# Kernel tuning notes

Measured on AMD Instinct MI355X. Metric: run time of the kernel, lower is better.

The kernel has to match this reference:

```python
import jax, jax.numpy as jnp
import numpy as np

B, H, L, DIM = 4, 8, 1024, 256
D = DIM // H  # per-head dim
DEPTH, LAYER_I = 12, 1  # layer_index < depth//4 -> adjacency masking active


def _gcn(xh, adj, W):
    # One graph-convolution layer (GCN used as q/k/v projection in the repo):
    # support = x @ W per head, then aggregate with the (attention-)adjacency.
    # xh: [b,h,t,d], adj: [b,h,l,t], W: [d,d] -> [b,h,l,d]
    return jnp.einsum('bhlt,bhtd->bhld', adj, xh @ W)


def _split_heads(x):
    # 'b t (h d) -> b h t d'
    b, t, _ = x.shape
    return x.reshape(b, t, H, D).transpose(0, 2, 1, 3)


def _merge_heads(v):
    # 'b h t d -> b t (h d)'
    b, h, t, d = v.shape
    return v.transpose(0, 2, 1, 3).reshape(b, t, h * d)


def setup_inputs() -> dict:
    key = jax.random.key(0)
    ks = jax.random.split(key, 9)
    x = jax.random.normal(ks[0], (B, L, DIM), jnp.float32)
    resize_x = jax.random.normal(ks[1], (B, L, DIM), jnpp := jnp.float32) if False else jax.random.normal(ks[1], (B, L, DIM), jnp.float32)
    eye = jnp.eye(L, dtype=jnp.float32)[None, None]  # self-loops so no all-masked rows
    adj = jnp.clip((jax.random.uniform(ks[2], (B, H, L, L)) < 0.1).astype(jnp.float32) + eye, 0.0, 1.0)
    adj_resize = jnp.clip((jax.random.uniform(ks[3], (B, H, L, L)) < 0.1).astype(jnp.float32) + eye, 0.0, 1.0)
    s = D ** -0.5
    Wq = jax.random.normal(ks[4], (D, D), jnp.float32) * s
    Wk = jax.random.normal(ks[5], (D, D), jnp.float32) * s
    Wv = jax.random.normal(ks[6], (D, D), jnp.float32) * s
    R = jax.random.normal(ks[7], (H, H), jnp.float32)  # 'randomatrix' head-mixing param
    Wp = jax.random.normal(ks[8], (DIM, DIM), jnp.float32) * (DIM ** -0.5)  # proj_v (no bias)
    return {'x': x, 'resize_x': resize_x, 'adj': adj, 'adj_resize': adj_resize,
            'Wq': Wq, 'Wk': Wk, 'Wv': Wv, 'R': R, 'Wp': Wp}


def reference(x, resize_x, adj, adj_resize, Wq, Wk, Wv, R, Wp):
    scale = DIM ** -0.5  # note: torch code scales by dim**-0.5 (full dim, not d_head)
    xh = _split_heads(x)          # [b,h,l,d]
    rxh = _split_heads(resize_x)  # [b,h,t,d]
    q = _gcn(xh, adj, Wq)         # [b,h,l,d]
    k = _gcn(rxh, adj_resize, Wk)  # [b,h,t,d]
    attn = jnp.einsum('bhld,bhtd->bhlt', q, k) * scale
    attn = jax.nn.leaky_relu(attn, negative_slope=0.01)
    # cross-head mixing with learned HxH matrix: out[b,i] = sum_h R[i,h]*attn[b,h]
    attn = jnp.einsum('ih,bhlt->bilt', R, attn)
    if LAYER_I < DEPTH // 4:
        attn = jnp.where(adj > 0, attn, -jnp.inf)
    A = jax.nn.softmax(attn, axis=-1)                      # rep_adj
    Ar = jax.nn.softmax(A.transpose(0, 1, 3, 2), axis=-1)  # dual softmax on transpose
    v = _merge_heads(_gcn(xh, A, Wv))
    out = jax.nn.gelu(v, approximate=False) @ Wp
    vr = _merge_heads(_gcn(rxh, Ar, Wv))
    out_resize = jax.nn.gelu(vr, approximate=False) @ Wp
    return out, out_resize, A, Ar
```

## Files before the change

### kernel.cpp

```cpp
#include <hip/hip_runtime.h>
#include <hip/hip_bf16.h>
#include <math.h>

#define BB 4
#define HH 8
#define LL 1024
#define DD 32
#define DIMM 256

typedef unsigned short u16;
typedef unsigned int u32;
typedef short bf16x8 __attribute__((ext_vector_type(8)));
typedef float f32x4 __attribute__((ext_vector_type(4)));

__device__ __forceinline__ float bu2f(u16 s) {
  union { unsigned int u; float f; } cv; cv.u = ((unsigned int)s) << 16; return cv.f;
}
__device__ __forceinline__ u16 f2bu(float f) {
  union { float f; unsigned int u; } cv; cv.f = f;
  unsigned int u = cv.u;
  u += 0x7FFFu + ((u >> 16) & 1u);
  return (u16)(u >> 16);
}
__device__ __forceinline__ short f2bs(float f) {
  return (short)__bfloat16_as_ushort(__float2bfloat16(f));
}

__global__ __launch_bounds__(256) void k_proj(
    const float* __restrict__ x, const float* __restrict__ rx,
    const float* __restrict__ Wq, const float* __restrict__ Wk, const float* __restrict__ Wv,
    u16* __restrict__ xqT_hi, u16* __restrict__ xqT_lo,
    u16* __restrict__ xkT_hi, u16* __restrict__ xkT_lo,
    u16* __restrict__ xvT_hi, u16* __restrict__ xvrT_hi) {
  __shared__ float wq[32][32], wk[32][32], wv[32][32];
  __shared__ float xs[8][32], rxs[8][32];
  __shared__ float tq_[32][9], tk_[32][9], tv_[32][9], tvr_[32][9];
  int tid = threadIdx.x, bid = blockIdx.x;
  int chunk = bid & 127, h = (bid >> 7) & 7, b = bid >> 10;
  int t0 = chunk << 3;
  for (int i = tid; i < 1024; i += 256) {
    int r = i >> 5, c = i & 31;
    wq[r][c] = Wq[i]; wk[r][c] = Wk[i]; wv[r][c] = Wv[i];
  }
  int d = tid & 31, tl = tid >> 5;
  size_t xoff = ((size_t)b * LL + t0 + tl) * DIMM + h * 32 + d;
  xs[tl][d]  = x[xoff];
  rxs[tl][d] = rx[xoff];
  __syncthreads();
  float aq = 0.f, ak = 0.f, av = 0.f, ar = 0.f;
#pragma unroll
  for (int dp = 0; dp < 32; ++dp) {
    float xv_ = xs[tl][dp], rv_ = rxs[tl][dp];
    aq += xv_ * wq[dp][d];
    ak += rv_ * wk[dp][d];
    av += xv_ * wv[dp][d];
    ar += rv_ * wv[dp][d];
  }
  tq_[d][tl] = aq; tk_[d][tl] = ak; tv_[d][tl] = av; tvr_[d][tl] = ar;
  __syncthreads();
  int d2 = tid >> 3, t2 = tid & 7;
  size_t obase = ((size_t)((b * HH + h) * DD + d2)) * LL + t0 + t2;
  {
    float v = tq_[d2][t2]; u16 hi = f2bu(v);
    xqT_hi[obase] = hi; xqT_lo[obase] = f2bu(v - bu2f(hi));
  }
  {
    float v = tk_[d2][t2]; u16 hi = f2bu(v);
    xkT_hi[obase] = hi; xkT_lo[obase] = f2bu(v - bu2f(hi));
  }
  xvT_hi[obase]  = f2bu(tv_[d2][t2]);
  xvrT_hi[obase] = f2bu(tvr_[d2][t2]);
}

template<int PREC, int OUT_SPLIT, int WRITE_BITS>
__global__ __launch_bounds__(256) void k_wmat2(
    const float* __restrict__ wA, const float* __restrict__ wB,
    const u16* __restrict__ sAh, const u16* __restrict__ sAl,
    const u16* __restrict__ sBh, const u16* __restrict__ sBl,
    float* __restrict__ dA, float* __restrict__ dB,
    u16* __restrict__ dAhi, u16* __restrict__ dAlo,
    u16* __restrict__ dBhi, u16* __restrict__ dBlo,
    u32* __restrict__ bits) {
  int tid = threadIdx.x, bid = blockIdx.x;
  int sel = bid >> 9;
  const float* w  = sel ? wB : wA;
  const u16* sh   = sel ? sBh : sAh;
  const u16* sl   = sel ? sBl : sAl;
  float* dst      = sel ? dB : dA;
  u16* dhi        = sel ? dBhi : dAhi;
  u16* dlo        = sel ? dBlo : dAlo;
  int b2 = bid & 511;
  int lc = b2 & 15, bh = b2 >> 4;
  int wave = tid >> 6, lane = tid & 63;
  int l0 = (lc << 6) + (wave << 4);
  int col = lane & 15, g = lane >> 4;
  const float* wrow = w + ((size_t)bh * LL + l0 + col) * LL + (g << 3);
  const u16* b0h = sh + ((size_t)bh * DD + col) * LL + (g << 3);
  const u16* b1h = b0h + 16 * LL;
  const u16* b0l = PREC == 2 ? sl + ((size_t)bh * DD + col) * LL + (g << 3) : nullptr;
  const u16* b1l = PREC == 2 ? b0l + 16 * LL : nullptr;
  unsigned char* bytep = nullptr;
  if (WRITE_BITS && sel == 0)
    bytep = (unsigned char*)(bits + (size_t)bh * 32 * LL + l0 + col) + g;
  f32x4 acc0 = {0.f, 0.f, 0.f, 0.f}, acc1 = {0.f, 0.f, 0.f, 0.f};
#pragma unroll 2
  for (int t0 = 0; t0 < LL; t0 += 32) {
    f32x4 wa = *(const f32x4*)(wrow + t0);
    f32x4 wb = *(const f32x4*)(wrow + t0 + 4);
    bf16x8 whi;
#pragma unroll
    for (int i = 0; i < 4; ++i) {
      whi[i]     = f2bs(wa[i]);
      whi[i + 4] = f2bs(wb[i]);
    }
    if (WRITE_BITS && sel == 0) {
      unsigned int byte = 0;
#pragma unroll
      for (int i = 0; i < 4; ++i) {
        byte |= (wa[i] > 0.f ? 1u : 0u) << i;
        byte |= (wb[i] > 0.f ? 1u : 0u) << (4 + i);
      }
      bytep[(size_t)(t0 >> 5) * (LL * 4)] = (unsigned char)byte;
    }
    bf16x8 s0h = *(const bf16x8*)(b0h + t0);
    bf16x8 s1h = *(const bf16x8*)(b1h + t0);
    acc0 = __builtin_amdgcn_mfma_f32_16x16x32_bf16(whi, s0h, acc0, 0, 0, 0);
    acc1 = __builtin_amdgcn_mfma_f32_16x16x32_bf16(whi, s1h, acc1, 0, 0, 0);
    if (PREC == 2) {
      bf16x8 s0l = *(const bf16x8*)(b0l + t0);
      bf16x8 s1l = *(const bf16x8*)(b1l + t0);
      acc0 = __builtin_amdgcn_mfma_f32_16x16x32_bf16(whi, s0l, acc0, 0, 0, 0);
      acc1 = __builtin_amdgcn_mfma_f32_16x16x32_bf16(whi, s1l, acc1, 0, 0, 0);
    }
  }
#pragma unroll
  for (int i = 0; i < 4; ++i) {
    size_t o = ((size_t)bh * LL + l0 + (g << 2) + i) * DD;
    if (OUT_SPLIT) {
      float v0 = acc0[i]; u16 h0 = f2bu(v0);
      dhi[o + col] = h0; dlo[o + col] = f2bu(v0 - bu2f(h0));
      float v1 = acc1[i]; u16 h1 = f2bu(v1);
      dhi[o + 16 + col] = h1; dlo[o + 16 + col] = f2bu(v1 - bu2f(h1));
    } else {
      dst[o + col] = acc0[i];
      dst[o + 16 + col] = acc1[i];
    }
  }
}

__global__ __launch_bounds__(256) void k_logits_mfma(
    const u16* __restrict__ qh, const u16* __restrict__ ql,
    const u16* __restrict__ kh, const u16* __restrict__ kl,
    const float* __restrict__ Rm, const u32* __restrict__ bits,
    float* __restrict__ M) {
  __shared__ float Rlds[8][8];
  __shared__ float mtile[4][16 * 17];
  int tid = threadIdx.x, bid = blockIdx.x;
  int tb = bid & 7, lb = (bid >> 3) & 15, b = bid >> 7;
  int wave = tid >> 6, lane = tid & 63;
  int l0 = (lb << 6) + (wave << 4);
  int tbase = tb << 7;
  int idx16 = lane & 15, g = lane >> 4;
  if (tid < 64) Rlds[tid >> 3][tid & 7] = Rm[tid];
  bf16x8 qfh[8], qfl[8];
#pragma unroll
  for (int h = 0; h < 8; ++h) {
    size_t off = ((size_t)(b * HH + h) * LL + l0 + idx16) * DD + (g << 3);
    qfh[h] = *(const bf16x8*)(qh + off);
    qfl[h] = *(const bf16x8*)(ql + off);
  }
  __syncthreads();
  int rr_ = lane >> 2, c0 = (lane & 3) << 2;
  for (int tt = 0; tt < 8; ++tt) {
    int t = tbase + (tt << 4);
    f32x4 S[8];
#pragma unroll
    for (int h = 0; h < 8; ++h) {
      size_t koff = ((size_t)(b * HH + h) * LL + t + idx16) * DD + (g << 3);
      bf16x8 bh_ = *(const bf16x8*)(kh + koff);
      bf16x8 bl_ = *(const bf16x8*)(kl + koff);
      f32x4 s = {0.f, 0.f, 0.f, 0.f};
      s = __builtin_amdgcn_mfma_f32_16x16x32_bf16(qfh[h], bh_, s, 0, 0, 0);
      s = __builtin_amdgcn_mfma_f32_16x16x32_bf16(qfl[h], bh_, s, 0, 0, 0);
      s = __builtin_amdgcn_mfma_f32_16x16x32_bf16(qfh[h], bl_, s, 0, 0, 0);
      S[h] = s;
    }
#pragma unroll
    for (int h = 0; h < 8; ++h)
#pragma unroll
      for (int e = 0; e < 4; ++e) {
        float v = S[h][e] * 0.0625f;
        S[h][e] = (v > 0.f) ? v : 0.01f * v;
      }
    int word = t >> 5;
    int bitpos = ((tt & 1) << 4) + idx16;
#pragma unroll
    for (int i = 0; i < 8; ++i) {
      float rr8[8];
#pragma unroll
      for (int h = 0; h < 8; ++h) rr8[h] = Rlds[i][h];
      const u32* bp = bits + ((size_t)(b * HH + i) * 32 + word) * LL + l0 + (g << 2);
      u32 mw0 = bp[0], mw1 = bp[1], mw2 = bp[2], mw3 = bp[3];
      float m_[4];
#pragma unroll
      for (int e = 0; e < 4; ++e) {
        float acc = 0.f;
#pragma unroll
        for (int h = 0; h < 8; ++h) acc += rr8[h] * S[h][e];
        u32 mw = (e == 0) ? mw0 : (e == 1) ? mw1 : (e == 2) ? mw2 : mw3;
        m_[e] = ((mw >> bitpos) & 1u) ? acc : -INFINITY;
      }
#pragma unroll
      for (int e = 0; e < 4; ++e)
        mtile[wave][((g << 2) + e) * 17 + idx16] = m_[e];
      float4 v4;
      v4.x = mtile[wave][rr_ * 17 + c0 + 0];
      v4.y = mtile[wave][rr_ * 17 + c0 + 1];
      v4.z = mtile[wave][rr_ * 17 + c0 + 2];
      v4.w = mtile[wave][rr_ * 17 + c0 + 3];
      *(float4*)(M + ((size_t)(b * HH + i) * LL + l0 + rr_) * LL + t + c0) = v4;
    }
  }
}

__global__ __launch_bounds__(256) void k_norm2(
    float* __restrict__ A, float* __restrict__ colpart) {
  __shared__ float cacc[4][1024];
  int tid = threadIdx.x, bid = blockIdx.x;
  int ch = bid & 31, bh = bid >> 5;
  int wave = tid >> 6, lane = tid & 63;
  float4 colA[4];
#pragma unroll
  for (int j = 0; j < 4; ++j) colA[j] = make_float4(0.f, 0.f, 0.f, 0.f);
  for (int rr = 0; rr < 8; ++rr) {
    int l = (ch << 5) + (rr << 2) + wave;
    float4* Ap = (float4*)(A + ((size_t)bh * LL + l) * LL);
    float4 v[4];
#pragma unroll
    for (int j = 0; j < 4; ++j) v[j] = Ap[lane + (j << 6)];
    float mx = -INFINITY;
#pragma unroll
    for (int j = 0; j < 4; ++j)
      mx = fmaxf(mx, fmaxf(fmaxf(v[j].x, v[j].y), fmaxf(v[j].z, v[j].w)));
#pragma unroll
    for (int o = 32; o > 0; o >>= 1) mx = fmaxf(mx, __shfl_xor(mx, o, 64));
    float sm = 0.f;
#pragma unroll
    for (int j = 0; j < 4; ++j) {
      v[j].x = __expf(v[j].x - mx); v[j].y = __expf(v[j].y - mx);
      v[j].z = __expf(v[j].z - mx); v[j].w = __expf(v[j].w - mx);
      sm += v[j].x + v[j].y + v[j].z + v[j].w;
    }
#pragma unroll
    for (int o = 32; o > 0; o >>= 1) sm += __shfl_xor(sm, o, 64);
    float inv = 1.0f / sm;
#pragma unroll
    for (int j = 0; j < 4; ++j) {
      v[j].x *= inv; v[j].y *= inv; v[j].z *= inv; v[j].w *= inv;
      colA[j].x += __expf(v[j].x); colA[j].y += __expf(v[j].y);
      colA[j].z += __expf(v[j].z); colA[j].w += __expf(v[j].w);
      Ap[lane + (j << 6)] = v[j];
    }
  }
#pragma unroll
  for (int j = 0; j < 4; ++j)
    *(float4*)&cacc[wave][(j << 8) + (lane << 2)] = colA[j];
  __syncthreads();
  float4 s = make_float4(0.f, 0.f, 0.f, 0.f);
#pragma unroll
  for (int w = 0; w < 4; ++w) {
    float4 t = *(const float4*)&cacc[w][tid << 2];
    s.x += t.x; s.y += t.y; s.z += t.z; s.w += t.w;
  }
  ((float4*)(colpart + ((size_t)bh * 32 + ch) * LL))[tid] = s;
}

__global__ __launch_bounds__(256) void k_colred(
    const float* __restrict__ colpart, float* __restrict__ colsum) {
  int gid = blockIdx.x * 256 + threadIdx.x;
  int bh = gid >> 10, t = gid & 1023;
  const float* cp = colpart + (size_t)bh * 32 * LL + t;
  float s = 0.f;
#pragma unroll
  for (int c = 0; c < 32; ++c) s += cp[c * LL];
  colsum[gid] = s;
}

__global__ __launch_bounds__(256) void k_ar(
    const float* __restrict__ A, const float* __restrict__ colsum, float* __restrict__ Ar) {
  __shared__ float tile[64][65];
  int tid = threadIdx.x, bid = blockIdx.x;
  int tix = bid & 15, tiy = (bid >> 4) & 15, bh = bid >> 8;
  int l0 = tiy << 6, t0 = tix << 6;
  int c = tid & 63, r4 = tid >> 6;
  const float* Ab = A + ((size_t)bh * LL + l0) * LL + t0;
#pragma unroll
  for (int rr = 0; rr < 16; ++rr) {
    int li = (rr << 2) + r4;
    tile[li][c] = __expf(Ab[(size_t)li * LL + c]);
  }
  __syncthreads();
  float* Arb = Ar + ((size_t)bh * LL + t0) * LL + l0;
  const float* cs = colsum + bh * LL + t0;
#pragma unroll
  for (int rr = 0; rr < 16; ++rr) {
    int ti = (rr << 2) + r4;
    float inv = 1.0f / cs[ti];
    Arb[(size_t)ti * LL + c] = tile[c][ti] * inv;
  }
}

__global__ __launch_bounds__(256) void k_out2(
    const float* __restrict__ vb, const float* __restrict__ vrb,
    const float* __restrict__ Wp,
    float* __restrict__ out, float* __restrict__ outr) {
  __shared__ float g_s[16 * 256];
  __shared__ float wp_s[32 * 256];
  int tid = threadIdx.x, bid = blockIdx.x;
  int sel = bid >> 8;
  const float* vbuf = sel ? vrb : vb;
  float* o = sel ? outr : out;
  int b2 = bid & 255;
  int lt = b2 & 63, b = b2 >> 6;
  int l0 = lt << 4;
  int h = tid >> 5, dd = tid & 31;
#pragma unroll
  for (int r = 0; r < 16; ++r) {
    float v = vbuf[(((size_t)b * HH + h) * LL + l0 + r) * DD + dd];
    g_s[r * 256 + tid] = 0.5f * v * (1.0f + erff(v * 0.70710678118654752f));
  }
  float acc[16];
#pragma unroll
  for (int r = 0; r < 16; ++r) acc[r] = 0.f;
  for (int jc = 0; jc < 8; ++jc) {
    __syncthreads();
#pragma unroll
    for (int u = 0; u < 8; ++u) {
      int idx = tid + (u << 8);
      int j = idx >> 6, c4 = idx & 63;
      float4 v = *(const float4*)(Wp + (size_t)(jc * 32 + j) * DIMM + (c4 << 2));
      *(float4*)&wp_s[j * 256 + (c4 << 2)] = v;
    }
    __syncthreads();
#pragma unroll
    for (int j = 0; j < 32; ++j) {
      float wv = wp_s[j * 256 + tid];
      int jj = (jc << 5) + j;
#pragma unroll
      for (int r = 0; r < 16; ++r)
        acc[r] += g_s[r * 256 + jj] * wv;
    }
  }
#pragma unroll
  for (int r = 0; r < 16; ++r)
    o[((size_t)b * LL + l0 + r) * DIMM + tid] = acc[r];
}

extern "C" void kernel_launch(void* const* d_in, const int* in_sizes, int n_in,
                              void* d_out, int out_size, void* d_ws, size_t ws_size,
                              hipStream_t stream) {
  const float* x    = (const float*)d_in[0];
  const float* rx   = (const float*)d_in[1];
  const float* adj  = (const float*)d_in[2];
  const float* adjr = (const float*)d_in[3];
  const float* Wq   = (const float*)d_in[4];
  const float* Wk   = (const float*)d_in[5];
  const float* Wv   = (const float*)d_in[6];
  const float* Rm   = (const float*)d_in[7];
  const float* Wp   = (const float*)d_in[8];

  const size_t NE = (size_t)BB * HH * LL * DD;

  float* out  = (float*)d_out;
  float* outr = out + NE;
  float* A    = outr + NE;
  float* Ar   = A + (size_t)BB * HH * LL * LL;

  float* colpart = Ar;
  u16* q_hi   = (u16*)(Ar + NE);
  u16* q_lo   = q_hi + NE;
  u16* k_hi   = q_lo + NE;
  u16* k_lo   = k_hi + NE;
  u16* xqT_hi = k_lo + NE;
  u16* xqT_lo = xqT_hi + NE;
  u16* xkT_hi = xqT_lo + NE;
  u16* xkT_lo = xkT_hi + NE;
  u16* xvT_hi  = (u16*)out;
  u16* xvrT_hi = (u16*)outr;

  float* wsf    = (float*)d_ws;
  float* vb     = wsf;
  float* vrb    = wsf + NE;
  float* colsum = wsf + 2 * NE;
  u32* adjbits  = (u32*)(wsf + 2 * NE + 32768);

  k_proj<<<4096, 256, 0, stream>>>(x, rx, Wq, Wk, Wv,
                                   xqT_hi, xqT_lo, xkT_hi, xkT_lo,
                                   xvT_hi, xvrT_hi);
  k_wmat2<2,1,1><<<1024, 256, 0, stream>>>(adj, adjr,
                                           xqT_hi, xqT_lo, xkT_hi, xkT_lo,
                                           nullptr, nullptr,
                                           q_hi, q_lo, k_hi, k_lo, adjbits);
  k_logits_mfma<<<512, 256, 0, stream>>>(q_hi, q_lo, k_hi, k_lo, Rm, adjbits, A);
  k_norm2<<<1024, 256, 0, stream>>>(A, colpart);
  k_colred<<<128, 256, 0, stream>>>(colpart, colsum);
  k_ar<<<8192, 256, 0, stream>>>(A, colsum, Ar);
  k_wmat2<1,0,0><<<1024, 256, 0, stream>>>(A, Ar,
                                           xvT_hi, nullptr, xvrT_hi, nullptr,
                                           vb, vrb,
                                           nullptr, nullptr, nullptr, nullptr, nullptr);
  k_out2<<<512, 256, 0, stream>>>(vb, vrb, Wp, out, outr);
}
```

Baseline: 423.4 us.

## Fuse value aggregation GEMMs into softmax-normalize and transpose kernels

```diff
diff --git a/kernel.cpp b/kernel.cpp
--- a/kernel.cpp
+++ b/kernel.cpp
@@ -223,9 +223,10 @@
   }
 }
 
-__global__ __launch_bounds__(256) void k_norm2(
-    float* __restrict__ A, float* __restrict__ colpart) {
-  __shared__ float cacc[4][1024];
+__global__ __launch_bounds__(256) void k_norm2v(
+    float* __restrict__ A, const u16* __restrict__ xvT,
+    float* __restrict__ colpart, float* __restrict__ vb) {
+  __shared__ u16 Ast[32][1032];
   int tid = threadIdx.x, bid = blockIdx.x;
   int ch = bid & 31, bh = bid >> 5;
   int wave = tid >> 6, lane = tid & 63;
@@ -233,7 +234,8 @@
 #pragma unroll
   for (int j = 0; j < 4; ++j) colA[j] = make_float4(0.f, 0.f, 0.f, 0.f);
   for (int rr = 0; rr < 8; ++rr) {
-    int l = (ch << 5) + (rr << 2) + wave;
+    int row = (rr << 2) + wave;
+    int l = (ch << 5) + row;
     float4* Ap = (float4*)(A + ((size_t)bh * LL + l) * LL);
     float4 v[4];
 #pragma unroll
@@ -260,16 +262,35 @@
       colA[j].x += __expf(v[j].x); colA[j].y += __expf(v[j].y);
       colA[j].z += __expf(v[j].z); colA[j].w += __expf(v[j].w);
       Ap[lane + (j << 6)] = v[j];
-    }
-  }
+      int c4 = (lane + (j << 6)) << 2;
+      *(short4*)&Ast[row][c4] =
+          make_short4(f2bs(v[j].x), f2bs(v[j].y), f2bs(v[j].z), f2bs(v[j].w));
+    }
+  }
+  __syncthreads();
+  int idx16 = lane & 15, g = lane >> 4;
+  int Mt = wave >> 1, Nt = wave & 1;
+  f32x4 acc = {0.f, 0.f, 0.f, 0.f};
+  const u16* bbase = xvT + ((size_t)bh * DD + Nt * 16 + idx16) * LL;
+#pragma unroll 4
+  for (int kc = 0; kc < 32; ++kc) {
+    bf16x8 af = *(const bf16x8*)&Ast[(Mt << 4) + idx16][(kc << 5) + (g << 3)];
+    bf16x8 bfr = *(const bf16x8*)(bbase + (kc << 5) + (g << 3));
+    acc = __builtin_amdgcn_mfma_f32_16x16x32_bf16(af, bfr, acc, 0, 0, 0);
+  }
+#pragma unroll
+  for (int e = 0; e < 4; ++e)
+    vb[((size_t)bh * LL + (ch << 5) + (Mt << 4) + (g << 2) + e) * DD + Nt * 16 + idx16] = acc[e];
+  __syncthreads();
+  float* cf = (float*)&Ast[0][0];
 #pragma unroll
   for (int j = 0; j < 4; ++j)
-    *(float4*)&cacc[wave][(j << 8) + (lane << 2)] = colA[j];
+    *(float4*)&cf[wave * 1024 + (j << 8) + (lane << 2)] = colA[j];
   __syncthreads();
   float4 s = make_float4(0.f, 0.f, 0.f, 0.f);
 #pragma unroll
   for (int w = 0; w < 4; ++w) {
-    float4 t = *(const float4*)&cacc[w][tid << 2];
+    float4 t = *(const float4*)&cf[w * 1024 + (tid << 2)];
     s.x += t.x; s.y += t.y; s.z += t.z; s.w += t.w;
   }
   ((float4*)(colpart + ((size_t)bh * 32 + ch) * LL))[tid] = s;
@@ -286,27 +307,51 @@
   colsum[gid] = s;
 }
 
-__global__ __launch_bounds__(256) void k_ar(
-    const float* __restrict__ A, const float* __restrict__ colsum, float* __restrict__ Ar) {
+__global__ __launch_bounds__(256) void k_arv(
+    const float* __restrict__ A, const float* __restrict__ colsum,
+    const u16* __restrict__ xvrT, float* __restrict__ Ar, float* __restrict__ vrb) {
   __shared__ float tile[64][65];
   int tid = threadIdx.x, bid = blockIdx.x;
-  int tix = bid & 15, tiy = (bid >> 4) & 15, bh = bid >> 8;
-  int l0 = tiy << 6, t0 = tix << 6;
-  int c = tid & 63, r4 = tid >> 6;
-  const float* Ab = A + ((size_t)bh * LL + l0) * LL + t0;
-#pragma unroll
-  for (int rr = 0; rr < 16; ++rr) {
-    int li = (rr << 2) + r4;
-    tile[li][c] = __expf(Ab[(size_t)li * LL + c]);
-  }
-  __syncthreads();
-  float* Arb = Ar + ((size_t)bh * LL + t0) * LL + l0;
-  const float* cs = colsum + bh * LL + t0;
-#pragma unroll
-  for (int rr = 0; rr < 16; ++rr) {
-    int ti = (rr << 2) + r4;
-    float inv = 1.0f / cs[ti];
-    Arb[(size_t)ti * LL + c] = tile[c][ti] * inv;
+  int tix = bid & 15, bh = bid >> 4;
+  int t0 = tix << 6;
+  int c = tid & 63, w4 = tid >> 6;
+  int idx16 = c & 15, g = (c >> 4) & 3;
+  float invc = 1.0f / colsum[(size_t)bh * LL + t0 + c];
+  f32x4 acc0 = {0.f, 0.f, 0.f, 0.f}, acc1 = {0.f, 0.f, 0.f, 0.f};
+  for (int tiy = 0; tiy < 16; ++tiy) {
+    int l0 = tiy << 6;
+    const float* Ab = A + ((size_t)bh * LL + l0) * LL + t0;
+#pragma unroll
+    for (int rr = 0; rr < 16; ++rr) {
+      int li = (rr << 2) + w4;
+      tile[li][c] = __expf(Ab[(size_t)li * LL + c]) * invc;
+    }
+    __syncthreads();
+    float* Arb = Ar + ((size_t)bh * LL + t0) * LL + l0;
+#pragma unroll
+    for (int rr = 0; rr < 16; ++rr) {
+      int ti = (rr << 2) + w4;
+      Arb[(size_t)ti * LL + c] = tile[c][ti];
+    }
+#pragma unroll
+    for (int kc = 0; kc < 2; ++kc) {
+      bf16x8 af;
+#pragma unroll
+      for (int j = 0; j < 8; ++j)
+        af[j] = f2bs(tile[(kc << 5) + (g << 3) + j][(w4 << 4) + idx16]);
+      const u16* bp = xvrT + ((size_t)bh * DD + idx16) * LL + l0 + (kc << 5) + (g << 3);
+      bf16x8 b0 = *(const bf16x8*)bp;
+      bf16x8 b1 = *(const bf16x8*)(bp + 16 * LL);
+      acc0 = __builtin_amdgcn_mfma_f32_16x16x32_bf16(af, b0, acc0, 0, 0, 0);
+      acc1 = __builtin_amdgcn_mfma_f32_16x16x32_bf16(af, b1, acc1, 0, 0, 0);
+    }
+    __syncthreads();
+  }
+#pragma unroll
+  for (int e = 0; e < 4; ++e) {
+    size_t o = ((size_t)bh * LL + t0 + (w4 << 4) + (g << 2) + e) * DD;
+    vrb[o + idx16] = acc0[e];
+    vrb[o + 16 + idx16] = acc1[e];
   }
 }
 
@@ -402,12 +447,8 @@
                                            nullptr, nullptr,
                                            q_hi, q_lo, k_hi, k_lo, adjbits);
   k_logits_mfma<<<512, 256, 0, stream>>>(q_hi, q_lo, k_hi, k_lo, Rm, adjbits, A);
-  k_norm2<<<1024, 256, 0, stream>>>(A, colpart);
+  k_norm2v<<<1024, 256, 0, stream>>>(A, xvT_hi, colpart, vb);
   k_colred<<<128, 256, 0, stream>>>(colpart, colsum);
-  k_ar<<<8192, 256, 0, stream>>>(A, colsum, Ar);
-  k_wmat2<1,0,0><<<1024, 256, 0, stream>>>(A, Ar,
-                                           xvT_hi, nullptr, xvrT_hi, nullptr,
-                                           vb, vrb,
-                                           nullptr, nullptr, nullptr, nullptr, nullptr);
+  k_arv<<<512, 256, 0, stream>>>(A, colsum, xvrT_hi, Ar, vrb);
   k_out2<<<512, 256, 0, stream>>>(vb, vrb, Wp, out, outr);
 }
```

New measurement: 399.7 us. 1.06x faster.
